# Kernel optimization log

Measured on AMD Instinct MI355X. Metric: run time of the kernel, lower is better.

The kernel has to match this reference:

```python
import jax, jax.numpy as jnp
import numpy as np

B, S, N_NODES, D_IN = 8, 24, 400, 3
D_MODEL = 32
G1_HEADS, G1_DIM = 4, 16
G2_HEADS, G2_DIM = 1, 32
T_KEY = 32


def _ln(x, g, b, eps=1e-6):
    m = jnp.mean(x, -1, keepdims=True)
    v = jnp.var(x, -1, keepdims=True)
    return g * (x - m) / jnp.sqrt(v + eps) + b


def _gat(x, adj, wq, bq, wk, bk, wv, bv, heads, dim):
    # x: [B*, N, F]; adjacency-masked multi-head attention (GraphAttention)
    Bx, N, _ = x.shape
    q = (x @ wq + bq).reshape(Bx, N, heads, dim)
    k = (x @ wk + bk).reshape(Bx, N, heads, dim)
    v = (x @ wv + bv).reshape(Bx, N, heads, dim)
    s = jnp.einsum('bihd,bjhd->bhij', q, k) / jnp.sqrt(jnp.float32(dim))
    s = jnp.where((adj == 0)[None, None], jnp.float32(-1e9), s)
    w = jax.nn.softmax(s, axis=-1)
    o = jnp.einsum('bhij,bjhd->bihd', w, v)
    return o.reshape(Bx, N, heads * dim)


def _mha(x, wq, bq, wk, bk, wv, bv, wo, bo):
    # keras MultiHeadAttention(num_heads=2, key_dim=32), self-attention, output dim = 32
    q = jnp.einsum('bsd,dhk->bshk', x, wq) + bq
    k = jnp.einsum('bsd,dhk->bshk', x, wk) + bk
    v = jnp.einsum('bsd,dhk->bshk', x, wv) + bv
    a = jax.nn.softmax(jnp.einsum('bqhk,bshk->bhqs', q, k) / jnp.sqrt(jnp.float32(T_KEY)), axis=-1)
    o = jnp.einsum('bhqs,bshk->bqhk', a, v)
    return jnp.einsum('bqhk,hko->bqo', o, wo) + bo


def setup_inputs() -> dict:
    ks = jax.random.split(jax.random.key(0), 20)

    def w(k, shape, scale=0.05):
        return (jax.random.normal(k, shape) * scale).astype(jnp.float32)

    z = lambda *s: jnp.zeros(s, jnp.float32)
    one = lambda *s: jnp.ones(s, jnp.float32)

    d = {}
    d['inputs'] = jax.random.normal(ks[0], (B, S, N_NODES, D_IN), dtype=jnp.float32)
    adj = (jax.random.uniform(ks[1], (N_NODES, N_NODES)) < 0.05).astype(jnp.float32)
    adj = jnp.minimum(adj + jnp.eye(N_NODES, dtype=jnp.float32), 1.0)
    d['adj'] = adj / (jnp.sum(adj, axis=1, keepdims=True) + 1e-6)  # row-normalized

    d['g1_wq'] = w(ks[2], (D_IN, G1_HEADS * G1_DIM)); d['g1_bq'] = z(G1_HEADS * G1_DIM)
    d['g1_wk'] = w(ks[3], (D_IN, G1_HEADS * G1_DIM)); d['g1_bk'] = z(G1_HEADS * G1_DIM)
    d['g1_wv'] = w(ks[4], (D_IN, G1_HEADS * G1_DIM)); d['g1_bv'] = z(G1_HEADS * G1_DIM)
    d['g2_wq'] = w(ks[5], (G1_HEADS * G1_DIM, G2_DIM)); d['g2_bq'] = z(G2_DIM)
    d['g2_wk'] = w(ks[6], (G1_HEADS * G1_DIM, G2_DIM)); d['g2_bk'] = z(G2_DIM)
    d['g2_wv'] = w(ks[7], (G1_HEADS * G1_DIM, G2_DIM)); d['g2_bv'] = z(G2_DIM)
    d['sp_g'] = one(D_MODEL); d['sp_b'] = z(D_MODEL)
    d['t_wq'] = w(ks[8], (D_MODEL, 2, T_KEY)); d['t_bq'] = z(2, T_KEY)
    d['t_wk'] = w(ks[9], (D_MODEL, 2, T_KEY)); d['t_bk'] = z(2, T_KEY)
    d['t_wv'] = w(ks[10], (D_MODEL, 2, T_KEY)); d['t_bv'] = z(2, T_KEY)
    d['t_wo'] = w(ks[11], (2, T_KEY, D_MODEL)); d['t_bo'] = z(D_MODEL)
    d['ff_w1'] = w(ks[12], (D_MODEL, 64)); d['ff_b1'] = z(64)
    d['ff_w2'] = w(ks[13], (64, D_MODEL)); d['ff_b2'] = z(D_MODEL)
    d['ln1_g'] = one(D_MODEL); d['ln1_b'] = z(D_MODEL)
    d['ln2_g'] = one(D_MODEL); d['ln2_b'] = z(D_MODEL)
    d['fin_g'] = one(D_MODEL); d['fin_b'] = z(D_MODEL)
    d['fd_w'] = w(ks[14], (D_MODEL, 1), scale=0.01); d['fd_b'] = z(1)
    return d


def reference(inputs, adj, g1_wq, g1_bq, g1_wk, g1_bk, g1_wv, g1_bv,
              g2_wq, g2_bq, g2_wk, g2_bk, g2_wv, g2_bv, sp_g, sp_b,
              t_wq, t_bq, t_wk, t_bk, t_wv, t_bv, t_wo, t_bo,
              ff_w1, ff_b1, ff_w2, ff_b2, ln1_g, ln1_b, ln2_g, ln2_b,
              fin_g, fin_b, fd_w, fd_b):
    Bx, Sx, N, _ = inputs.shape
    x = inputs.reshape(Bx * Sx, N, D_IN)

    # SpatialProcessor: GAT1 -> relu -> GAT2 -> residual layernorm
    h = jax.nn.relu(_gat(x, adj, g1_wq, g1_bq, g1_wk, g1_bk, g1_wv, g1_bv, G1_HEADS, G1_DIM))
    h = _gat(h, adj, g2_wq, g2_bq, g2_wk, g2_bk, g2_wv, g2_bv, G2_HEADS, G2_DIM)
    res = jnp.pad(x, ((0, 0), (0, 0), (0, D_MODEL - D_IN)))  # zero-pad 3 -> 32 for residual
    sp = _ln(h + res, sp_g, sp_b)
    sp4 = sp.reshape(Bx, Sx, N, D_MODEL)  # [B, S, N, 32]

    # TemporalTransformer over sequence per node
    t_in = jnp.transpose(sp4, (0, 2, 1, 3)).reshape(Bx * N, Sx, D_MODEL)
    a = _mha(t_in, t_wq, t_bq, t_wk, t_bk, t_wv, t_bv, t_wo, t_bo)
    x1 = _ln(t_in + a, ln1_g, ln1_b)
    f = jax.nn.gelu(x1 @ ff_w1 + ff_b1, approximate=False) @ ff_w2 + ff_b2
    t_out = _ln(x1 + f, ln2_g, ln2_b).reshape(Bx, N, Sx, D_MODEL)

    # fuse: mean over seq (spatial) + mean over seq (temporal), layernorm, final dense
    fused = _ln(jnp.mean(sp4, axis=1) + jnp.mean(t_out, axis=2), fin_g, fin_b)
    return (fused @ fd_w + fd_b)[..., 0]  # [B, N]
```

## Files before the change

### kernel.cpp

```cpp
#include <hip/hip_runtime.h>
#include <hip/hip_bf16.h>

#define NN 400
#define KMAX 64

struct WTab {
  const void* p[34];
  int off[35];
};

__device__ __forceinline__ float bflo(unsigned u) {
  union { unsigned i; float f; } x; x.i = u << 16; return x.f;
}
__device__ __forceinline__ float bfhi(unsigned u) {
  union { unsigned i; float f; } x; x.i = u & 0xffff0000u; return x.f;
}
__device__ __forceinline__ unsigned short f2bf(float f) {
  __hip_bfloat16 b = __float2bfloat16(f);
  return *reinterpret_cast<unsigned short*>(&b);
}
__device__ __forceinline__ unsigned packbf(float a, float b) {
  return (unsigned)f2bf(a) | ((unsigned)f2bf(b) << 16);
}
__device__ __forceinline__ bool detect_bf16(const unsigned short* probe) {
  int lane = threadIdx.x & 63;
  unsigned short u = probe[lane * 2];
  int e = (u >> 7) & 0xFF;
  bool plaus = (u == 0) || (e >= 112 && e <= 132);
  return __popcll(__ballot(plaus)) >= 48;
}
__device__ __forceinline__ float rsum32(float v) {
  v += __shfl_xor(v, 1); v += __shfl_xor(v, 2); v += __shfl_xor(v, 4);
  v += __shfl_xor(v, 8); v += __shfl_xor(v, 16); return v;
}

__global__ __launch_bounds__(256) void prep_k(
    WTab wt, const void* __restrict__ adj,
    const unsigned short* __restrict__ probe, float* __restrict__ dst,
    int* __restrict__ colp, int* __restrict__ degp) {
  bool isbf = detect_bf16(probe);
  const int tid = threadIdx.x;
  if (blockIdx.x < 40) {
    int total = wt.off[34];
    for (int i = blockIdx.x * 256 + tid; i < total; i += 40 * 256) {
      int lo = 0, hi = 33;
      while (lo < hi) {
        int mid = (lo + hi + 1) >> 1;
        if (i >= wt.off[mid]) lo = mid; else hi = mid - 1;
      }
      int rel = i - wt.off[lo];
      float v;
      if (isbf) v = __bfloat162float(((const __hip_bfloat16*)wt.p[lo])[rel]);
      else      v = ((const float*)wt.p[lo])[rel];
      dst[i] = v;
    }
  } else {
    int row = (blockIdx.x - 40) * 4 + (tid >> 6);
    int lane = tid & 63;
    int base = 0;
    for (int j0 = 0; j0 < NN; j0 += 64) {
      int j = j0 + lane;
      bool nz;
      if (isbf) nz = (j < NN) && ((const unsigned short*)adj)[row * NN + j] != 0;
      else      nz = (j < NN) && ((const float*)adj)[row * NN + j] != 0.0f;
      unsigned long long m = __ballot(nz);
      int offl = __popcll(m & ((1ull << lane) - 1ull));
      if (nz) {
        int pidx = base + offl;
        if (pidx < KMAX) colp[row * KMAX + pidx] = j;
      }
      base += __popcll(m);
    }
    if (lane == 0) degp[row] = base < KMAX ? base : KMAX;
  }
}

__global__ __launch_bounds__(256) void gat1_k(
    const void* __restrict__ xraw, const unsigned short* __restrict__ probe,
    const float* __restrict__ g1, const int* __restrict__ colp,
    const int* __restrict__ degp, unsigned short* __restrict__ h1b) {
  __shared__ float xsf[NN * 4];
  __shared__ float yhf[4 * NN * 4];
  __shared__ float w1s[768];
  __shared__ float cf[64];
  const int tid = threadIdx.x;
  const int g = blockIdx.x;
  bool isbf = detect_bf16(probe);

  for (int e = tid; e < 768; e += 256) w1s[e] = g1[e];
  for (int e = tid; e < NN; e += 256) xsf[e * 4 + 3] = 0.f;
  for (int e = tid; e < NN * 3; e += 256) {
    int j = e / 3, a = e - j * 3;
    float v;
    if (isbf) v = __bfloat162float(((const __hip_bfloat16*)xraw)[g * NN * 3 + e]);
    else      v = ((const float*)xraw)[g * NN * 3 + e];
    xsf[j * 4 + a] = v;
  }
  __syncthreads();

  if (tid < 64) {
    int h = tid >> 4, t = tid & 15, co = h * 16;
    float acc = 0.f;
    if (t < 9) {
      int a = t / 3, b = t - (t / 3) * 3;
      for (int c = 0; c < 16; ++c) acc += w1s[a * 64 + co + c] * w1s[256 + b * 64 + co + c];
    } else if (t < 12) {
      int a = t - 9;
      for (int c = 0; c < 16; ++c) acc += w1s[a * 64 + co + c] * w1s[448 + co + c];
    } else if (t < 15) {
      int b = t - 12;
      for (int c = 0; c < 16; ++c) acc += w1s[256 + b * 64 + co + c] * w1s[192 + co + c];
    } else {
      for (int c = 0; c < 16; ++c) acc += w1s[192 + co + c] * w1s[448 + co + c];
    }
    cf[h * 16 + t] = acc;
  }
  __syncthreads();

  for (int e = tid; e < NN * 4; e += 256) {
    int j = e >> 2, h = e & 3;
    const float* bse = cf + h * 16;
    float x0 = xsf[j * 4], x1 = xsf[j * 4 + 1], x2 = xsf[j * 4 + 2];
    float* y = yhf + (h * NN + j) * 4;
    y[0] = bse[0] * x0 + bse[1] * x1 + bse[2] * x2;
    y[1] = bse[3] * x0 + bse[4] * x1 + bse[5] * x2;
    y[2] = bse[6] * x0 + bse[7] * x1 + bse[8] * x2;
    y[3] = bse[12] * x0 + bse[13] * x1 + bse[14] * x2 + bse[15];
  }
  __syncthreads();

  const float4* xs4 = (const float4*)xsf;
  const float4* yh4 = (const float4*)yhf;
  const int i0 = blockIdx.y * 200;
  for (int i = i0 + tid; i < i0 + 200; i += 256) {
    float4 xi = xs4[i];
    float ch[4];
    #pragma unroll
    for (int h = 0; h < 4; ++h)
      ch[h] = cf[h * 16 + 9] * xi.x + cf[h * 16 + 10] * xi.y + cf[h * 16 + 11] * xi.z;
    float l[4] = {0.f, 0.f, 0.f, 0.f};
    float ax[4], ay[4], az[4];
    #pragma unroll
    for (int h = 0; h < 4; ++h) { ax[h] = 0.f; ay[h] = 0.f; az[h] = 0.f; }
    int dg = degp[i];
    const int* cols = colp + i * KMAX;
    for (int e = 0; e < dg; ++e) {
      int j = cols[e];
      float4 xj = xs4[j];
      #pragma unroll
      for (int h = 0; h < 4; ++h) {
        float4 y = yh4[h * NN + j];
        float s = (xi.x * y.x + xi.y * y.y + xi.z * y.z + y.w + ch[h]) * 0.25f;
        float p = __expf(s);
        l[h] += p;
        ax[h] += p * xj.x; ay[h] += p * xj.y; az[h] += p * xj.z;
      }
    }
    unsigned* hr = (unsigned*)(h1b + ((size_t)g * NN + i) * 64);
    #pragma unroll
    for (int h = 0; h < 4; ++h) {
      float inv = 1.f / l[h];
      float b0 = ax[h] * inv, b1 = ay[h] * inv, b2 = az[h] * inv;
      int co = h * 16;
      #pragma unroll
      for (int c = 0; c < 16; c += 2) {
        float o0 = fmaxf(b0 * w1s[512 + co + c] + b1 * w1s[576 + co + c] +
                         b2 * w1s[640 + co + c] + w1s[704 + co + c], 0.f);
        float o1 = fmaxf(b0 * w1s[513 + co + c] + b1 * w1s[577 + co + c] +
                         b2 * w1s[641 + co + c] + w1s[705 + co + c], 0.f);
        hr[(co + c) >> 1] = packbf(o0, o1);
      }
    }
  }
}

__global__ __launch_bounds__(256) void gat2_proj_k(
    const unsigned short* __restrict__ h1b, const float* __restrict__ g2,
    unsigned short* __restrict__ q2b, unsigned short* __restrict__ k2g,
    unsigned short* __restrict__ v2g) {
  __shared__ float ht[64 * 68];
  const int tid = threadIdx.x, t = blockIdx.x;
  for (int e = tid; e < 2048; e += 256) {
    unsigned u = ((const unsigned*)h1b)[t * 2048 + e];
    int ln = e >> 5, d0 = (e & 31) * 2;
    ht[d0 * 68 + ln] = bflo(u);
    ht[(d0 + 1) * 68 + ln] = bfhi(u);
  }
  __syncthreads();
  const int c = tid & 31, ng = tid >> 5;
  const float* wq = g2;
  const float* wk = g2 + 2080;
  const float* wv = g2 + 4160;
  float qa[8], ka[8], va[8];
  float bq = g2[2048 + c], bk = g2[4128 + c], bv = g2[6208 + c];
  #pragma unroll
  for (int k = 0; k < 8; ++k) { qa[k] = bq; ka[k] = bk; va[k] = bv; }
  for (int d = 0; d < 64; ++d) {
    float wqv = wq[d * 32 + c], wkv = wk[d * 32 + c], wvv = wv[d * 32 + c];
    const float4* hp = (const float4*)(ht + d * 68 + ng * 8);
    float4 h0 = hp[0], h1v = hp[1];
    float hv[8] = {h0.x, h0.y, h0.z, h0.w, h1v.x, h1v.y, h1v.z, h1v.w};
    #pragma unroll
    for (int k = 0; k < 8; ++k) {
      qa[k] += hv[k] * wqv; ka[k] += hv[k] * wkv; va[k] += hv[k] * wvv;
    }
  }
  #pragma unroll
  for (int k = 0; k < 8; ++k) {
    int gn = t * 64 + ng * 8 + k;
    q2b[gn * 32 + c] = f2bf(qa[k]);
    k2g[gn * 32 + c] = f2bf(ka[k]);
    v2g[gn * 32 + c] = f2bf(va[k]);
  }
}

__global__ __launch_bounds__(256) void gat2_attn_k(
    const void* __restrict__ xraw, const unsigned short* __restrict__ probe,
    const unsigned short* __restrict__ q2b, const unsigned short* __restrict__ k2g,
    const unsigned short* __restrict__ v2g, const float* __restrict__ spw,
    const int* __restrict__ colp, const int* __restrict__ degp,
    float* __restrict__ spo) {
  __shared__ unsigned short k2s[NN * 40];
  __shared__ unsigned short v2s[NN * 40];
  __shared__ float gw[64];
  const int tid = threadIdx.x;
  const int g = blockIdx.x;
  bool isbf = detect_bf16(probe);
  if (tid < 64) gw[tid] = spw[tid];
  for (int e = tid; e < 6400; e += 256) {
    unsigned uk = ((const unsigned*)k2g)[g * 6400 + e];
    unsigned uv = ((const unsigned*)v2g)[g * 6400 + e];
    int n = e >> 4, c = e & 15;
    ((unsigned*)k2s)[n * 20 + c] = uk;
    ((unsigned*)v2s)[n * 20 + c] = uv;
  }
  __syncthreads();
  const int b = g / 24, st = g % 24;
  const int i0 = blockIdx.y * 200;
  for (int i = i0 + tid; i < i0 + 200; i += 256) {
    const uint4* qp = (const uint4*)(q2b + ((size_t)g * NN + i) * 32);
    uint4 qw[4] = {qp[0], qp[1], qp[2], qp[3]};
    float q[32], o[32];
    #pragma unroll
    for (int t = 0; t < 4; ++t) {
      unsigned uu[4] = {qw[t].x, qw[t].y, qw[t].z, qw[t].w};
      #pragma unroll
      for (int m = 0; m < 4; ++m) {
        q[t * 8 + 2 * m] = bflo(uu[m]); q[t * 8 + 2 * m + 1] = bfhi(uu[m]);
      }
    }
    #pragma unroll
    for (int c = 0; c < 32; ++c) o[c] = 0.f;
    int dg = degp[i];
    const int* cols = colp + i * KMAX;
    float l = 0.f;
    for (int e = 0; e < dg; ++e) {
      int j = cols[e];
      const uint4* kr = (const uint4*)(k2s + j * 40);
      const uint4* vr = (const uint4*)(v2s + j * 40);
      float s = 0.f;
      #pragma unroll
      for (int t = 0; t < 4; ++t) {
        uint4 kk = kr[t];
        unsigned uu[4] = {kk.x, kk.y, kk.z, kk.w};
        #pragma unroll
        for (int m = 0; m < 4; ++m)
          s += q[t * 8 + 2 * m] * bflo(uu[m]) + q[t * 8 + 2 * m + 1] * bfhi(uu[m]);
      }
      float p = __expf(s * 0.17677669529663688f);
      l += p;
      #pragma unroll
      for (int t = 0; t < 4; ++t) {
        uint4 vv = vr[t];
        unsigned uu[4] = {vv.x, vv.y, vv.z, vv.w};
        #pragma unroll
        for (int m = 0; m < 4; ++m) {
          o[t * 8 + 2 * m]     += p * bflo(uu[m]);
          o[t * 8 + 2 * m + 1] += p * bfhi(uu[m]);
        }
      }
    }
    float inv = 1.f / l;
    float xr[3];
    #pragma unroll
    for (int a = 0; a < 3; ++a) {
      if (isbf) xr[a] = __bfloat162float(((const __hip_bfloat16*)xraw)[((size_t)g * NN + i) * 3 + a]);
      else      xr[a] = ((const float*)xraw)[((size_t)g * NN + i) * 3 + a];
    }
    float row[32];
    #pragma unroll
    for (int c = 0; c < 32; ++c) row[c] = o[c] * inv;
    row[0] += xr[0]; row[1] += xr[1]; row[2] += xr[2];
    float mean = 0.f;
    #pragma unroll
    for (int c = 0; c < 32; ++c) mean += row[c];
    mean *= (1.f / 32.f);
    float var = 0.f;
    #pragma unroll
    for (int c = 0; c < 32; ++c) { float dd = row[c] - mean; var += dd * dd; }
    var *= (1.f / 32.f);
    float rinv = 1.f / sqrtf(var + 1e-6f);
    float4* so4 = (float4*)(spo + (((size_t)b * NN + i) * 24 + st) * 32);
    #pragma unroll
    for (int k = 0; k < 8; ++k) {
      float4 v;
      v.x = gw[4 * k]     * (row[4 * k]     - mean) * rinv + gw[32 + 4 * k];
      v.y = gw[4 * k + 1] * (row[4 * k + 1] - mean) * rinv + gw[33 + 4 * k];
      v.z = gw[4 * k + 2] * (row[4 * k + 2] - mean) * rinv + gw[34 + 4 * k];
      v.w = gw[4 * k + 3] * (row[4 * k + 3] - mean) * rinv + gw[35 + 4 * k];
      so4[k] = v;
    }
  }
}

__global__ __launch_bounds__(128) void temporal_k(
    const float* __restrict__ sp, const float* __restrict__ tw,
    const unsigned short* __restrict__ probe, void* __restrict__ outp) {
  __shared__ float sm[7472];
  float* t_s = sm;
  float* q_s = sm + 768;
  float* k_s = sm + 2328;
  float* v_s = sm + 3888;
  float* aw  = sm + 5448;
  float* x1s = sm + 6648;
  float* red = sm + 7440;
  float* att = q_s;
  float* f1s = k_s;
  float* tos = v_s;
  const int tid = threadIdx.x;
  bool isbf = detect_bf16(probe);

  const float* twq = tw;            const float* tbq = tw + 2048;
  const float* twk = tw + 2112;     const float* tbk = tw + 4160;
  const float* twv = tw + 4224;     const float* tbv = tw + 6272;
  const float* two = tw + 6336;     const float* tbo = tw + 8384;
  const float* fw1 = tw + 8416;     const float* fb1 = tw + 10464;
  const float* fw2 = tw + 10528;    const float* fb2 = tw + 12576;
  const float* l1g = tw + 12608;    const float* l1b = tw + 12640;
  const float* l2g = tw + 12672;    const float* l2b = tw + 12704;
  const float* fng = tw + 12736;    const float* fnb = tw + 12768;
  const float* fdw = tw + 12800;    const float* fdb = tw + 12832;

  const float4* base4 = (const float4*)(sp + (size_t)blockIdx.x * 768);
  for (int e = tid; e < 192; e += 128) ((float4*)t_s)[e] = base4[e];
  __syncthreads();

  {
    const int hk = tid & 63, sh = tid >> 6;
    for (int a = 0; a < 3; ++a) {
      const float* W  = (a == 0) ? twq : (a == 1) ? twk : twv;
      const float* Bb = (a == 0) ? tbq : (a == 1) ? tbk : tbv;
      float* dst      = (a == 0) ? q_s : (a == 1) ? k_s : v_s;
      float w[32];
      #pragma unroll
      for (int c = 0; c < 32; ++c) w[c] = W[c * 64 + hk];
      float bias = Bb[hk];
      for (int s = sh * 12; s < sh * 12 + 12; ++s) {
        float acc = bias;
        const float* tr = t_s + s * 32;
        #pragma unroll
        for (int c = 0; c < 32; ++c) acc += tr[c] * w[c];
        dst[s * 65 + hk] = acc;
      }
    }
  }
  __syncthreads();

  if (tid < 96) {
    const int h = tid / 48, rem = tid % 48, qs = rem >> 1, half = rem & 1;
    const float* qr = q_s + qs * 65 + h * 32;
    float sc[12], l = 0.f;
    #pragma unroll
    for (int k = 0; k < 12; ++k) {
      const float* kr = k_s + (half * 12 + k) * 65 + h * 32;
      float s = 0.f;
      #pragma unroll
      for (int d = 0; d < 32; ++d) s += qr[d] * kr[d];
      sc[k] = __expf(s * 0.17677669529663688f);
      l += sc[k];
    }
    l += __shfl_xor(l, 1);
    float inv = 1.f / l;
    float* ar = aw + (h * 24 + qs) * 25 + half * 12;
    #pragma unroll
    for (int k = 0; k < 12; ++k) ar[k] = sc[k] * inv;
  }
  __syncthreads();

  for (int e = tid; e < 1536; e += 128) {
    int qs = e >> 6, hk = e & 63, h = hk >> 5;
    const float* ar = aw + (h * 24 + qs) * 25;
    float a = 0.f;
    #pragma unroll
    for (int ss = 0; ss < 24; ++ss) a += ar[ss] * v_s[ss * 65 + hk];
    att[qs * 65 + hk] = a;
  }
  __syncthreads();

  for (int e = tid; e < 768; e += 128) {
    int s = e >> 5, c = e & 31;
    const float* ar = att + s * 65;
    float a = tbo[c];
    #pragma unroll 8
    for (int hk = 0; hk < 64; ++hk) a += ar[hk] * two[hk * 32 + c];
    x1s[s * 33 + c] = t_s[e] + a;
  }
  __syncthreads();
  if (tid < 24) {
    float* r = x1s + tid * 33;
    float mean = 0.f;
    for (int c = 0; c < 32; ++c) mean += r[c];
    mean *= (1.f / 32.f);
    float var = 0.f;
    for (int c = 0; c < 32; ++c) { float d = r[c] - mean; var += d * d; }
    var *= (1.f / 32.f);
    float ri = 1.f / sqrtf(var + 1e-6f);
    for (int c = 0; c < 32; ++c) r[c] = l1g[c] * (r[c] - mean) * ri + l1b[c];
  }
  __syncthreads();

  {
    const int j = tid & 63, sh = tid >> 6;
    float w[32];
    #pragma unroll
    for (int c = 0; c < 32; ++c) w[c] = fw1[c * 64 + j];
    float bias = fb1[j];
    for (int s = sh * 12; s < sh * 12 + 12; ++s) {
      float acc = bias;
      const float* xr = x1s + s * 33;
      #pragma unroll
      for (int c = 0; c < 32; ++c) acc += xr[c] * w[c];
      f1s[s * 64 + j] = 0.5f * acc * (1.f + erff(acc * 0.70710678118654752f));
    }
  }
  __syncthreads();

  for (int e = tid; e < 768; e += 128) {
    int s = e >> 5, c = e & 31;
    const float* fr = f1s + s * 64;
    float a = fb2[c];
    #pragma unroll 8
    for (int j = 0; j < 64; ++j) a += fr[j] * fw2[j * 32 + c];
    tos[s * 33 + c] = x1s[s * 33 + c] + a;
  }
  __syncthreads();
  if (tid < 24) {
    float* r = tos + tid * 33;
    float mean = 0.f;
    for (int c = 0; c < 32; ++c) mean += r[c];
    mean *= (1.f / 32.f);
    float var = 0.f;
    for (int c = 0; c < 32; ++c) { float d = r[c] - mean; var += d * d; }
    var *= (1.f / 32.f);
    float ri = 1.f / sqrtf(var + 1e-6f);
    for (int c = 0; c < 32; ++c) r[c] = l2g[c] * (r[c] - mean) * ri + l2b[c];
  }
  __syncthreads();

  if (tid < 32) {
    float ms = 0.f, mt = 0.f;
    for (int s = 0; s < 24; ++s) { ms += t_s[s * 32 + tid]; mt += tos[s * 33 + tid]; }
    red[tid] = (ms + mt) * (1.f / 24.f);
  }
  __syncthreads();
  if (tid == 0) {
    float mean = 0.f;
    for (int c = 0; c < 32; ++c) mean += red[c];
    mean *= (1.f / 32.f);
    float var = 0.f;
    for (int c = 0; c < 32; ++c) { float d = red[c] - mean; var += d * d; }
    var *= (1.f / 32.f);
    float ri = 1.f / sqrtf(var + 1e-6f);
    float acc = fdb[0];
    for (int c = 0; c < 32; ++c)
      acc += (fng[c] * (red[c] - mean) * ri + fnb[c]) * fdw[c];
    if (isbf) ((__hip_bfloat16*)outp)[blockIdx.x] = __float2bfloat16(acc);
    else      ((float*)outp)[blockIdx.x] = acc;
  }
}

extern "C" void kernel_launch(void* const* d_in, const int* in_sizes, int n_in,
                              void* d_out, int out_size, void* d_ws, size_t ws_size,
                              hipStream_t stream) {
  static const int wsizes[34] = {
      192, 64, 192, 64, 192, 64,
      2048, 32, 2048, 32, 2048, 32,
      32, 32,
      2048, 64, 2048, 64, 2048, 64, 2048, 32,
      2048, 64, 2048, 32,
      32, 32, 32, 32, 32, 32,
      32, 1};
  WTab wt;
  int off = 0;
  for (int i = 0; i < 34; ++i) { wt.p[i] = d_in[i + 2]; wt.off[i] = off; off += wsizes[i]; }
  wt.off[34] = off;

  char* ws = (char*)d_ws;
  float* convw = (float*)ws;
  int*   colp  = (int*)(ws + 81920);
  int*   degp  = (int*)(ws + 184320);
  unsigned short* h1b = (unsigned short*)(ws + 196608);
  float*          spo = (float*)(ws + 196608);
  unsigned short* q2b = (unsigned short*)(ws + 10027008);
  unsigned short* k2g = (unsigned short*)(ws + 14942208);
  unsigned short* v2g = (unsigned short*)(ws + 19857408);

  const float* g1  = convw;
  const float* g2  = convw + 768;
  const float* spw = convw + 7008;
  const float* twp = convw + 7072;
  const unsigned short* probe = (const unsigned short*)d_in[0];

  hipLaunchKernelGGL(prep_k, dim3(140), dim3(256), 0, stream, wt, d_in[1], probe,
                     convw, colp, degp);
  hipLaunchKernelGGL(gat1_k, dim3(192, 2), dim3(256), 0, stream, d_in[0], probe,
                     g1, (const int*)colp, (const int*)degp, h1b);
  hipLaunchKernelGGL(gat2_proj_k, dim3(1200), dim3(256), 0, stream,
                     (const unsigned short*)h1b, g2, q2b, k2g, v2g);
  hipLaunchKernelGGL(gat2_attn_k, dim3(192, 2), dim3(256), 0, stream, d_in[0],
                     probe, (const unsigned short*)q2b, (const unsigned short*)k2g,
                     (const unsigned short*)v2g, spw, (const int*)colp,
                     (const int*)degp, spo);
  hipLaunchKernelGGL(temporal_k, dim3(3200), dim3(128), 0, stream,
                     (const float*)spo, twp, probe, d_out);
}
```

Baseline: 312.7 us.

## Fuse GAT1, GAT2 projection and GAT2 attention into one spatial kernel

Merges the three spatial kernels into one block per graph (192 blocks). GAT1 output, the Q/K/V projections and the GAT2 attention now stay in registers and LDS, so the h1/q/k/v round-trips through global memory disappear. The precomputed per-head yh table is also dropped and recomputed per edge. In exchange, grid parallelism falls from 384+1200 blocks to 192 with launch_bounds(256,1), and each thread holds large register arrays (qreg[2][32] plus accumulators), which risks spills and low occupancy.

New measurement: 579.5 us. 1.85x slower.

```diff
diff --git a/kernel.cpp b/kernel.cpp
--- a/kernel.cpp
+++ b/kernel.cpp
@@ -28,10 +28,6 @@
   int e = (u >> 7) & 0xFF;
   bool plaus = (u == 0) || (e >= 112 && e <= 132);
   return __popcll(__ballot(plaus)) >= 48;
-}
-__device__ __forceinline__ float rsum32(float v) {
-  v += __shfl_xor(v, 1); v += __shfl_xor(v, 2); v += __shfl_xor(v, 4);
-  v += __shfl_xor(v, 8); v += __shfl_xor(v, 16); return v;
 }
 
 __global__ __launch_bounds__(256) void prep_k(
@@ -75,14 +71,16 @@
   }
 }
 
-__global__ __launch_bounds__(256) void gat1_k(
+__global__ __launch_bounds__(256, 1) void spatial_k(
     const void* __restrict__ xraw, const unsigned short* __restrict__ probe,
-    const float* __restrict__ g1, const int* __restrict__ colp,
-    const int* __restrict__ degp, unsigned short* __restrict__ h1b) {
+    const float* __restrict__ g1, const float* __restrict__ g2,
+    const float* __restrict__ spw, const int* __restrict__ colp,
+    const int* __restrict__ degp, float* __restrict__ spo) {
   __shared__ float xsf[NN * 4];
-  __shared__ float yhf[4 * NN * 4];
   __shared__ float w1s[768];
   __shared__ float cf[64];
+  __shared__ unsigned short k2s[NN * 34];
+  __shared__ unsigned short v2s[NN * 34];
   const int tid = threadIdx.x;
   const int g = blockIdx.x;
   bool isbf = detect_bf16(probe);
@@ -117,198 +115,153 @@
   }
   __syncthreads();
 
-  for (int e = tid; e < NN * 4; e += 256) {
-    int j = e >> 2, h = e & 3;
-    const float* bse = cf + h * 16;
-    float x0 = xsf[j * 4], x1 = xsf[j * 4 + 1], x2 = xsf[j * 4 + 2];
-    float* y = yhf + (h * NN + j) * 4;
-    y[0] = bse[0] * x0 + bse[1] * x1 + bse[2] * x2;
-    y[1] = bse[3] * x0 + bse[4] * x1 + bse[5] * x2;
-    y[2] = bse[6] * x0 + bse[7] * x1 + bse[8] * x2;
-    y[3] = bse[12] * x0 + bse[13] * x1 + bse[14] * x2 + bse[15];
-  }
-  __syncthreads();
-
   const float4* xs4 = (const float4*)xsf;
-  const float4* yh4 = (const float4*)yhf;
-  const int i0 = blockIdx.y * 200;
-  for (int i = i0 + tid; i < i0 + 200; i += 256) {
-    float4 xi = xs4[i];
-    float ch[4];
-    #pragma unroll
-    for (int h = 0; h < 4; ++h)
-      ch[h] = cf[h * 16 + 9] * xi.x + cf[h * 16 + 10] * xi.y + cf[h * 16 + 11] * xi.z;
-    float l[4] = {0.f, 0.f, 0.f, 0.f};
-    float ax[4], ay[4], az[4];
-    #pragma unroll
-    for (int h = 0; h < 4; ++h) { ax[h] = 0.f; ay[h] = 0.f; az[h] = 0.f; }
-    int dg = degp[i];
-    const int* cols = colp + i * KMAX;
-    for (int e = 0; e < dg; ++e) {
-      int j = cols[e];
-      float4 xj = xs4[j];
+  float qreg[2][32];
+  float xi0[2], xi1[2], xi2[2];
+
+  #pragma unroll
+  for (int pass = 0; pass < 2; ++pass) {
+    int i = tid + pass * 256;
+    if (i < NN) {
+      float4 xi = xs4[i];
+      xi0[pass] = xi.x; xi1[pass] = xi.y; xi2[pass] = xi.z;
+      float ch[4];
+      #pragma unroll
+      for (int h = 0; h < 4; ++h)
+        ch[h] = cf[h * 16 + 9] * xi.x + cf[h * 16 + 10] * xi.y + cf[h * 16 + 11] * xi.z;
+      float l[4], bx[4], by[4], bz[4];
+      #pragma unroll
+      for (int h = 0; h < 4; ++h) { l[h] = 0.f; bx[h] = 0.f; by[h] = 0.f; bz[h] = 0.f; }
+      int dg = degp[i];
+      const int* cols = colp + i * KMAX;
+      for (int e = 0; e < dg; ++e) {
+        int j = cols[e];
+        float4 xj = xs4[j];
+        #pragma unroll
+        for (int h = 0; h < 4; ++h) {
+          const float* M = cf + h * 16;
+          float y0 = M[0] * xj.x + M[1] * xj.y + M[2] * xj.z;
+          float y1 = M[3] * xj.x + M[4] * xj.y + M[5] * xj.z;
+          float y2 = M[6] * xj.x + M[7] * xj.y + M[8] * xj.z;
+          float dv = M[12] * xj.x + M[13] * xj.y + M[14] * xj.z + M[15];
+          float s = (xi.x * y0 + xi.y * y1 + xi.z * y2 + dv + ch[h]) * 0.25f;
+          float p = __expf(s);
+          l[h] += p;
+          bx[h] += p * xj.x; by[h] += p * xj.y; bz[h] += p * xj.z;
+        }
+      }
       #pragma unroll
       for (int h = 0; h < 4; ++h) {
-        float4 y = yh4[h * NN + j];
-        float s = (xi.x * y.x + xi.y * y.y + xi.z * y.z + y.w + ch[h]) * 0.25f;
-        float p = __expf(s);
-        l[h] += p;
-        ax[h] += p * xj.x; ay[h] += p * xj.y; az[h] += p * xj.z;
-      }
-    }
-    unsigned* hr = (unsigned*)(h1b + ((size_t)g * NN + i) * 64);
-    #pragma unroll
-    for (int h = 0; h < 4; ++h) {
-      float inv = 1.f / l[h];
-      float b0 = ax[h] * inv, b1 = ay[h] * inv, b2 = az[h] * inv;
-      int co = h * 16;
-      #pragma unroll
-      for (int c = 0; c < 16; c += 2) {
-        float o0 = fmaxf(b0 * w1s[512 + co + c] + b1 * w1s[576 + co + c] +
-                         b2 * w1s[640 + co + c] + w1s[704 + co + c], 0.f);
-        float o1 = fmaxf(b0 * w1s[513 + co + c] + b1 * w1s[577 + co + c] +
-                         b2 * w1s[641 + co + c] + w1s[705 + co + c], 0.f);
-        hr[(co + c) >> 1] = packbf(o0, o1);
-      }
-    }
-  }
-}
-
-__global__ __launch_bounds__(256) void gat2_proj_k(
-    const unsigned short* __restrict__ h1b, const float* __restrict__ g2,
-    unsigned short* __restrict__ q2b, unsigned short* __restrict__ k2g,
-    unsigned short* __restrict__ v2g) {
-  __shared__ float ht[64 * 68];
-  const int tid = threadIdx.x, t = blockIdx.x;
-  for (int e = tid; e < 2048; e += 256) {
-    unsigned u = ((const unsigned*)h1b)[t * 2048 + e];
-    int ln = e >> 5, d0 = (e & 31) * 2;
-    ht[d0 * 68 + ln] = bflo(u);
-    ht[(d0 + 1) * 68 + ln] = bfhi(u);
-  }
-  __syncthreads();
-  const int c = tid & 31, ng = tid >> 5;
-  const float* wq = g2;
-  const float* wk = g2 + 2080;
-  const float* wv = g2 + 4160;
-  float qa[8], ka[8], va[8];
-  float bq = g2[2048 + c], bk = g2[4128 + c], bv = g2[6208 + c];
+        float inv = 1.f / l[h];
+        bx[h] *= inv; by[h] *= inv; bz[h] *= inv;
+      }
+      #pragma unroll
+      for (int c = 0; c < 32; ++c) qreg[pass][c] = g2[2048 + c];
+      #pragma unroll
+      for (int h = 0; h < 4; ++h) {
+        for (int d2 = 0; d2 < 16; ++d2) {
+          int d = h * 16 + d2;
+          float hd = fmaxf(bx[h] * w1s[512 + d] + by[h] * w1s[576 + d] +
+                           bz[h] * w1s[640 + d] + w1s[704 + d], 0.f);
+          #pragma unroll
+          for (int c = 0; c < 32; ++c) qreg[pass][c] += hd * g2[d * 32 + c];
+        }
+      }
+      {
+        float acc[32];
+        #pragma unroll
+        for (int c = 0; c < 32; ++c) acc[c] = g2[4128 + c];
+        #pragma unroll
+        for (int h = 0; h < 4; ++h) {
+          for (int d2 = 0; d2 < 16; ++d2) {
+            int d = h * 16 + d2;
+            float hd = fmaxf(bx[h] * w1s[512 + d] + by[h] * w1s[576 + d] +
+                             bz[h] * w1s[640 + d] + w1s[704 + d], 0.f);
+            #pragma unroll
+            for (int c = 0; c < 32; ++c) acc[c] += hd * g2[2080 + d * 32 + c];
+          }
+        }
+        unsigned* kr = (unsigned*)(k2s + i * 34);
+        #pragma unroll
+        for (int m = 0; m < 16; ++m) kr[m] = packbf(acc[2 * m], acc[2 * m + 1]);
+      }
+      {
+        float acc[32];
+        #pragma unroll
+        for (int c = 0; c < 32; ++c) acc[c] = g2[6208 + c];
+        #pragma unroll
+        for (int h = 0; h < 4; ++h) {
+          for (int d2 = 0; d2 < 16; ++d2) {
+            int d = h * 16 + d2;
+            float hd = fmaxf(bx[h] * w1s[512 + d] + by[h] * w1s[576 + d] +
+                             bz[h] * w1s[640 + d] + w1s[704 + d], 0.f);
+            #pragma unroll
+            for (int c = 0; c < 32; ++c) acc[c] += hd * g2[4160 + d * 32 + c];
+          }
+        }
+        unsigned* vr = (unsigned*)(v2s + i * 34);
+        #pragma unroll
+        for (int m = 0; m < 16; ++m) vr[m] = packbf(acc[2 * m], acc[2 * m + 1]);
+      }
+    }
+  }
+  __syncthreads();
+
+  const int b = g / 24, st = g % 24;
+  const float rs32 = 0.17677669529663688f;
   #pragma unroll
-  for (int k = 0; k < 8; ++k) { qa[k] = bq; ka[k] = bk; va[k] = bv; }
-  for (int d = 0; d < 64; ++d) {
-    float wqv = wq[d * 32 + c], wkv = wk[d * 32 + c], wvv = wv[d * 32 + c];
-    const float4* hp = (const float4*)(ht + d * 68 + ng * 8);
-    float4 h0 = hp[0], h1v = hp[1];
-    float hv[8] = {h0.x, h0.y, h0.z, h0.w, h1v.x, h1v.y, h1v.z, h1v.w};
-    #pragma unroll
-    for (int k = 0; k < 8; ++k) {
-      qa[k] += hv[k] * wqv; ka[k] += hv[k] * wkv; va[k] += hv[k] * wvv;
-    }
-  }
-  #pragma unroll
-  for (int k = 0; k < 8; ++k) {
-    int gn = t * 64 + ng * 8 + k;
-    q2b[gn * 32 + c] = f2bf(qa[k]);
-    k2g[gn * 32 + c] = f2bf(ka[k]);
-    v2g[gn * 32 + c] = f2bf(va[k]);
-  }
-}
-
-__global__ __launch_bounds__(256) void gat2_attn_k(
-    const void* __restrict__ xraw, const unsigned short* __restrict__ probe,
-    const unsigned short* __restrict__ q2b, const unsigned short* __restrict__ k2g,
-    const unsigned short* __restrict__ v2g, const float* __restrict__ spw,
-    const int* __restrict__ colp, const int* __restrict__ degp,
-    float* __restrict__ spo) {
-  __shared__ unsigned short k2s[NN * 40];
-  __shared__ unsigned short v2s[NN * 40];
-  __shared__ float gw[64];
-  const int tid = threadIdx.x;
-  const int g = blockIdx.x;
-  bool isbf = detect_bf16(probe);
-  if (tid < 64) gw[tid] = spw[tid];
-  for (int e = tid; e < 6400; e += 256) {
-    unsigned uk = ((const unsigned*)k2g)[g * 6400 + e];
-    unsigned uv = ((const unsigned*)v2g)[g * 6400 + e];
-    int n = e >> 4, c = e & 15;
-    ((unsigned*)k2s)[n * 20 + c] = uk;
-    ((unsigned*)v2s)[n * 20 + c] = uv;
-  }
-  __syncthreads();
-  const int b = g / 24, st = g % 24;
-  const int i0 = blockIdx.y * 200;
-  for (int i = i0 + tid; i < i0 + 200; i += 256) {
-    const uint4* qp = (const uint4*)(q2b + ((size_t)g * NN + i) * 32);
-    uint4 qw[4] = {qp[0], qp[1], qp[2], qp[3]};
-    float q[32], o[32];
-    #pragma unroll
-    for (int t = 0; t < 4; ++t) {
-      unsigned uu[4] = {qw[t].x, qw[t].y, qw[t].z, qw[t].w};
-      #pragma unroll
-      for (int m = 0; m < 4; ++m) {
-        q[t * 8 + 2 * m] = bflo(uu[m]); q[t * 8 + 2 * m + 1] = bfhi(uu[m]);
-      }
-    }
-    #pragma unroll
-    for (int c = 0; c < 32; ++c) o[c] = 0.f;
-    int dg = degp[i];
-    const int* cols = colp + i * KMAX;
-    float l = 0.f;
-    for (int e = 0; e < dg; ++e) {
-      int j = cols[e];
-      const uint4* kr = (const uint4*)(k2s + j * 40);
-      const uint4* vr = (const uint4*)(v2s + j * 40);
-      float s = 0.f;
-      #pragma unroll
-      for (int t = 0; t < 4; ++t) {
-        uint4 kk = kr[t];
-        unsigned uu[4] = {kk.x, kk.y, kk.z, kk.w};
-        #pragma unroll
-        for (int m = 0; m < 4; ++m)
-          s += q[t * 8 + 2 * m] * bflo(uu[m]) + q[t * 8 + 2 * m + 1] * bfhi(uu[m]);
-      }
-      float p = __expf(s * 0.17677669529663688f);
-      l += p;
-      #pragma unroll
-      for (int t = 0; t < 4; ++t) {
-        uint4 vv = vr[t];
-        unsigned uu[4] = {vv.x, vv.y, vv.z, vv.w};
-        #pragma unroll
-        for (int m = 0; m < 4; ++m) {
-          o[t * 8 + 2 * m]     += p * bflo(uu[m]);
-          o[t * 8 + 2 * m + 1] += p * bfhi(uu[m]);
-        }
-      }
-    }
-    float inv = 1.f / l;
-    float xr[3];
-    #pragma unroll
-    for (int a = 0; a < 3; ++a) {
-      if (isbf) xr[a] = __bfloat162float(((const __hip_bfloat16*)xraw)[((size_t)g * NN + i) * 3 + a]);
-      else      xr[a] = ((const float*)xraw)[((size_t)g * NN + i) * 3 + a];
-    }
-    float row[32];
-    #pragma unroll
-    for (int c = 0; c < 32; ++c) row[c] = o[c] * inv;
-    row[0] += xr[0]; row[1] += xr[1]; row[2] += xr[2];
-    float mean = 0.f;
-    #pragma unroll
-    for (int c = 0; c < 32; ++c) mean += row[c];
-    mean *= (1.f / 32.f);
-    float var = 0.f;
-    #pragma unroll
-    for (int c = 0; c < 32; ++c) { float dd = row[c] - mean; var += dd * dd; }
-    var *= (1.f / 32.f);
-    float rinv = 1.f / sqrtf(var + 1e-6f);
-    float4* so4 = (float4*)(spo + (((size_t)b * NN + i) * 24 + st) * 32);
-    #pragma unroll
-    for (int k = 0; k < 8; ++k) {
-      float4 v;
-      v.x = gw[4 * k]     * (row[4 * k]     - mean) * rinv + gw[32 + 4 * k];
-      v.y = gw[4 * k + 1] * (row[4 * k + 1] - mean) * rinv + gw[33 + 4 * k];
-      v.z = gw[4 * k + 2] * (row[4 * k + 2] - mean) * rinv + gw[34 + 4 * k];
-      v.w = gw[4 * k + 3] * (row[4 * k + 3] - mean) * rinv + gw[35 + 4 * k];
-      so4[k] = v;
+  for (int pass = 0; pass < 2; ++pass) {
+    int i = tid + pass * 256;
+    if (i < NN) {
+      float o[32];
+      #pragma unroll
+      for (int c = 0; c < 32; ++c) o[c] = 0.f;
+      int dg = degp[i];
+      const int* cols = colp + i * KMAX;
+      float l = 0.f;
+      for (int e = 0; e < dg; ++e) {
+        int j = cols[e];
+        const unsigned* kr = (const unsigned*)(k2s + j * 34);
+        float s = 0.f;
+        #pragma unroll
+        for (int m = 0; m < 16; ++m) {
+          unsigned u = kr[m];
+          s += qreg[pass][2 * m] * bflo(u) + qreg[pass][2 * m + 1] * bfhi(u);
+        }
+        float p = __expf(s * rs32);
+        l += p;
+        const unsigned* vr = (const unsigned*)(v2s + j * 34);
+        #pragma unroll
+        for (int m = 0; m < 16; ++m) {
+          unsigned u = vr[m];
+          o[2 * m]     += p * bflo(u);
+          o[2 * m + 1] += p * bfhi(u);
+        }
+      }
+      float inv = 1.f / l;
+      float row[32];
+      #pragma unroll
+      for (int c = 0; c < 32; ++c) row[c] = o[c] * inv;
+      row[0] += xi0[pass]; row[1] += xi1[pass]; row[2] += xi2[pass];
+      float mean = 0.f;
+      #pragma unroll
+      for (int c = 0; c < 32; ++c) mean += row[c];
+      mean *= (1.f / 32.f);
+      float var = 0.f;
+      #pragma unroll
+      for (int c = 0; c < 32; ++c) { float dd = row[c] - mean; var += dd * dd; }
+      var *= (1.f / 32.f);
+      float rinv = 1.f / sqrtf(var + 1e-6f);
+      float4* so4 = (float4*)(spo + (((size_t)b * NN + i) * 24 + st) * 32);
+      #pragma unroll
+      for (int k = 0; k < 8; ++k) {
+        float4 v;
+        v.x = spw[4 * k]     * (row[4 * k]     - mean) * rinv + spw[32 + 4 * k];
+        v.y = spw[4 * k + 1] * (row[4 * k + 1] - mean) * rinv + spw[33 + 4 * k];
+        v.z = spw[4 * k + 2] * (row[4 * k + 2] - mean) * rinv + spw[34 + 4 * k];
+        v.w = spw[4 * k + 3] * (row[4 * k + 3] - mean) * rinv + spw[35 + 4 * k];
+        so4[k] = v;
+      }
     }
   }
 }
@@ -499,11 +452,7 @@
   float* convw = (float*)ws;
   int*   colp  = (int*)(ws + 81920);
   int*   degp  = (int*)(ws + 184320);
-  unsigned short* h1b = (unsigned short*)(ws + 196608);
-  float*          spo = (float*)(ws + 196608);
-  unsigned short* q2b = (unsigned short*)(ws + 10027008);
-  unsigned short* k2g = (unsigned short*)(ws + 14942208);
-  unsigned short* v2g = (unsigned short*)(ws + 19857408);
+  float* spo   = (float*)(ws + 196608);
 
   const float* g1  = convw;
   const float* g2  = convw + 768;
@@ -513,14 +462,8 @@
 
   hipLaunchKernelGGL(prep_k, dim3(140), dim3(256), 0, stream, wt, d_in[1], probe,
                      convw, colp, degp);
-  hipLaunchKernelGGL(gat1_k, dim3(192, 2), dim3(256), 0, stream, d_in[0], probe,
-                     g1, (const int*)colp, (const int*)degp, h1b);
-  hipLaunchKernelGGL(gat2_proj_k, dim3(1200), dim3(256), 0, stream,
-                     (const unsigned short*)h1b, g2, q2b, k2g, v2g);
-  hipLaunchKernelGGL(gat2_attn_k, dim3(192, 2), dim3(256), 0, stream, d_in[0],
-                     probe, (const unsigned short*)q2b, (const unsigned short*)k2g,
-                     (const unsigned short*)v2g, spw, (const int*)colp,
-                     (const int*)degp, spo);
+  hipLaunchKernelGGL(spatial_k, dim3(192), dim3(256), 0, stream, d_in[0], probe,
+                     g1, g2, spw, (const int*)colp, (const int*)degp, spo);
   hipLaunchKernelGGL(temporal_k, dim3(3200), dim3(128), 0, stream,
                      (const float*)spo, twp, probe, d_out);
 }
```

## Split GAT2 attention rows further, vectorize K/V staging, warp-reduce final layernorm

Applied to the files above, without the earlier changes.

The GAT2 attention grid goes from 2 to 4 row-chunks per graph, so each block handles 100 nodes. This doubles the number of blocks to spread across CUs, but every block still stages the full K/V tile and many threads sit idle. K/V staging now copies uint2 instead of 32-bit words. The temporal kernel shrinks its shared memory by aliasing x1s onto the attention-weight region and dropping the reduction buffer. Its final mean/layernorm/dense step becomes a 32-lane shuffle reduction in place of a single-thread serial loop.

Result: slower. 319.5 us (+2.2%).

```diff
diff --git a/kernel.cpp b/kernel.cpp
--- a/kernel.cpp
+++ b/kernel.cpp
@@ -227,17 +227,17 @@
   const int g = blockIdx.x;
   bool isbf = detect_bf16(probe);
   if (tid < 64) gw[tid] = spw[tid];
-  for (int e = tid; e < 6400; e += 256) {
-    unsigned uk = ((const unsigned*)k2g)[g * 6400 + e];
-    unsigned uv = ((const unsigned*)v2g)[g * 6400 + e];
-    int n = e >> 4, c = e & 15;
-    ((unsigned*)k2s)[n * 20 + c] = uk;
-    ((unsigned*)v2s)[n * 20 + c] = uv;
+  for (int e = tid; e < 3200; e += 256) {
+    uint2 uk = ((const uint2*)k2g)[g * 3200 + e];
+    uint2 uv = ((const uint2*)v2g)[g * 3200 + e];
+    int n = e >> 3, c = (e & 7) * 2;
+    *(uint2*)((unsigned*)k2s + n * 20 + c) = uk;
+    *(uint2*)((unsigned*)v2s + n * 20 + c) = uv;
   }
   __syncthreads();
   const int b = g / 24, st = g % 24;
-  const int i0 = blockIdx.y * 200;
-  for (int i = i0 + tid; i < i0 + 200; i += 256) {
+  const int i0 = blockIdx.y * 100;
+  for (int i = i0 + tid; i < i0 + 100; i += 256) {
     const uint4* qp = (const uint4*)(q2b + ((size_t)g * NN + i) * 32);
     uint4 qw[4] = {qp[0], qp[1], qp[2], qp[3]};
     float q[32], o[32];
@@ -316,14 +316,13 @@
 __global__ __launch_bounds__(128) void temporal_k(
     const float* __restrict__ sp, const float* __restrict__ tw,
     const unsigned short* __restrict__ probe, void* __restrict__ outp) {
-  __shared__ float sm[7472];
+  __shared__ float sm[6648];
   float* t_s = sm;
   float* q_s = sm + 768;
   float* k_s = sm + 2328;
   float* v_s = sm + 3888;
   float* aw  = sm + 5448;
-  float* x1s = sm + 6648;
-  float* red = sm + 7440;
+  float* x1s = sm + 5448;
   float* att = q_s;
   float* f1s = k_s;
   float* tos = v_s;
@@ -458,24 +457,22 @@
   __syncthreads();
 
   if (tid < 32) {
+    const int c = tid;
     float ms = 0.f, mt = 0.f;
-    for (int s = 0; s < 24; ++s) { ms += t_s[s * 32 + tid]; mt += tos[s * 33 + tid]; }
-    red[tid] = (ms + mt) * (1.f / 24.f);
-  }
-  __syncthreads();
-  if (tid == 0) {
-    float mean = 0.f;
-    for (int c = 0; c < 32; ++c) mean += red[c];
-    mean *= (1.f / 32.f);
-    float var = 0.f;
-    for (int c = 0; c < 32; ++c) { float d = red[c] - mean; var += d * d; }
-    var *= (1.f / 32.f);
+    #pragma unroll
+    for (int s = 0; s < 24; ++s) { ms += t_s[s * 32 + c]; mt += tos[s * 33 + c]; }
+    float red = (ms + mt) * (1.f / 24.f);
+    float mean = rsum32(red) * (1.f / 32.f);
+    float dv = red - mean;
+    float var = rsum32(dv * dv) * (1.f / 32.f);
     float ri = 1.f / sqrtf(var + 1e-6f);
-    float acc = fdb[0];
-    for (int c = 0; c < 32; ++c)
-      acc += (fng[c] * (red[c] - mean) * ri + fnb[c]) * fdw[c];
-    if (isbf) ((__hip_bfloat16*)outp)[blockIdx.x] = __float2bfloat16(acc);
-    else      ((float*)outp)[blockIdx.x] = acc;
+    float y = (fng[c] * dv * ri + fnb[c]) * fdw[c];
+    float tot = rsum32(y);
+    if (c == 0) {
+      float acc = tot + fdb[0];
+      if (isbf) ((__hip_bfloat16*)outp)[blockIdx.x] = __float2bfloat16(acc);
+      else      ((float*)outp)[blockIdx.x] = acc;
+    }
   }
 }
 
@@ -517,7 +514,7 @@
                      g1, (const int*)colp, (const int*)degp, h1b);
   hipLaunchKernelGGL(gat2_proj_k, dim3(1200), dim3(256), 0, stream,
                      (const unsigned short*)h1b, g2, q2b, k2g, v2g);
-  hipLaunchKernelGGL(gat2_attn_k, dim3(192, 2), dim3(256), 0, stream, d_in[0],
+  hipLaunchKernelGGL(gat2_attn_k, dim3(192, 4), dim3(256), 0, stream, d_in[0],
                      probe, (const unsigned short*)q2b, (const unsigned short*)k2g,
                      (const unsigned short*)v2g, spw, (const int*)colp,
                      (const int*)degp, spo);
```
